# Performance work log

Hardware: AMD Instinct MI355X
Metric: run time of the kernel (lower is better)

## Reference

```python
import jax, jax.numpy as jnp
import numpy as np
import math

B, T, INP_DIM, OUT_DIM = 2, 4096, 1, 64
DEPTH, D_MODEL, N_HEADS, D_FF = 4, 512, 8, 2048
D_HEAD = D_MODEL // N_HEADS
EPS = 1e-5


def setup_inputs() -> dict:
    key = jax.random.key(0)
    ks = jax.random.split(key, 16)
    s = 0.02
    inp = {
        "x_in": jax.random.normal(ks[0], (B, T, INP_DIM), dtype=jnp.float32),
        "inp_w": jax.random.normal(ks[1], (INP_DIM, D_MODEL), dtype=jnp.float32) * s,
        "inp_b": jnp.zeros((D_MODEL,), dtype=jnp.float32),
        "pos_emb": jax.random.normal(ks[2], (T, D_MODEL), dtype=jnp.float32) * s,
        "ln1_g": jnp.ones((DEPTH, D_MODEL), dtype=jnp.float32),
        "ln1_b": jnp.zeros((DEPTH, D_MODEL), dtype=jnp.float32),
        "qkv_w": jax.random.normal(ks[3], (DEPTH, D_MODEL, 3 * D_MODEL), dtype=jnp.float32) * s,
        "proj_w": jax.random.normal(ks[4], (DEPTH, D_MODEL, D_MODEL), dtype=jnp.float32) * s,
        "ln2_g": jnp.ones((DEPTH, D_MODEL), dtype=jnp.float32),
        "ln2_b": jnp.zeros((DEPTH, D_MODEL), dtype=jnp.float32),
        "fc1_w": jax.random.normal(ks[5], (DEPTH, D_MODEL, D_FF), dtype=jnp.float32) * s,
        "fc2_w": jax.random.normal(ks[6], (DEPTH, D_FF, D_MODEL), dtype=jnp.float32) * s,
        "lnf_g": jnp.ones((D_MODEL,), dtype=jnp.float32),
        "lnf_b": jnp.zeros((D_MODEL,), dtype=jnp.float32),
        "head_w": jax.random.normal(ks[7], (D_MODEL, OUT_DIM), dtype=jnp.float32) * s,
        "head_b": jnp.zeros((OUT_DIM,), dtype=jnp.float32),
    }
    return inp


def _layernorm(x, g, b):
    mu = jnp.mean(x, axis=-1, keepdims=True)
    var = jnp.mean(jnp.square(x - mu), axis=-1, keepdims=True)
    return (x - mu) * jax.lax.rsqrt(var + EPS) * g + b


def _attn(x, qkv_w, proj_w):
    Bx, Tx, d = x.shape
    qkv = x @ qkv_w  # [B,T,3d]
    q, k, v = jnp.split(qkv, 3, axis=-1)
    q = q.reshape(Bx, Tx, N_HEADS, D_HEAD)
    k = k.reshape(Bx, Tx, N_HEADS, D_HEAD)
    v = v.reshape(Bx, Tx, N_HEADS, D_HEAD)
    scores = jnp.einsum('bqhd,bkhd->bhqk', q, k) / math.sqrt(D_HEAD)
    causal = jnp.tril(jnp.ones((Tx, Tx), dtype=bool))
    scores = jnp.where(causal, scores, -jnp.inf)
    attn = jax.nn.softmax(scores, axis=-1)
    out = jnp.einsum('bhqk,bkhd->bqhd', attn, v).reshape(Bx, Tx, d)
    return out @ proj_w


def reference(x_in, inp_w, inp_b, pos_emb, ln1_g, ln1_b, qkv_w, proj_w,
              ln2_g, ln2_b, fc1_w, fc2_w, lnf_g, lnf_b, head_w, head_b):
    x = x_in @ inp_w + inp_b + pos_emb[None, :, :]  # [B,T,d]
    for l in range(DEPTH):
        x = x + _attn(_layernorm(x, ln1_g[l], ln1_b[l]), qkv_w[l], proj_w[l])
        h = _layernorm(x, ln2_g[l], ln2_b[l])
        h = jax.nn.gelu(h @ fc1_w[l], approximate=False) @ fc2_w[l]
        x = x + h
    h = _layernorm(x, lnf_g, lnf_b)
    return h @ head_w + head_b  # [B,T,out_dim]
```

## Files before the change

### kernel.cpp

```cpp
#include <hip/hip_runtime.h>
#include <math.h>

typedef unsigned short u16;
typedef unsigned int u32;

#define B_ 2
#define T_ 4096
#define DM 512
#define NH 8
#define DH 64
#define DFF 2048
#define MTOT (B_*T_)

#define SCALEQ 0.18033688011112042f

using f32x4  = __attribute__((ext_vector_type(4))) float;
using f32x16 = __attribute__((ext_vector_type(16))) float;
using bf16x8 = __attribute__((ext_vector_type(8))) short;

__device__ __forceinline__ float b2f(u16 u) {
  union { u32 u; float f; } v; v.u = ((u32)u) << 16; return v.f;
}
__device__ __forceinline__ u16 f2b(float f) {
  union { float f; u32 u; } v; v.f = f;
  u32 r = v.u + 0x7FFFu + ((v.u >> 16) & 1u);
  return (u16)(r >> 16);
}
__device__ __forceinline__ u32 cvtpk(float lo, float hi) {
  u32 r;
  asm("v_cvt_pk_bf16_f32 %0, %1, %2" : "=v"(r) : "v"(lo), "v"(hi));
  return r;
}
#if __has_builtin(__builtin_amdgcn_exp2f)
#define EXP2(x) __builtin_amdgcn_exp2f(x)
#else
#define EXP2(x) __expf((x) * 0.6931471805599453f)
#endif
#if __has_builtin(__builtin_amdgcn_rcpf)
#define RCP(x) __builtin_amdgcn_rcpf(x)
#else
#define RCP(x) (1.0f / (x))
#endif

__device__ __forceinline__ void gload_lds(const u16* g, u16* l) {
  __builtin_amdgcn_global_load_lds(
      (const __attribute__((address_space(1))) void*)g,
      (__attribute__((address_space(3))) void*)l, 16, 0, 0);
}

__device__ __forceinline__ int lsw(int row, int col) {
  int slot = ((col >> 3) + (row >> 3) + 2 * (row & 7)) & 7;
  return (row << 6) + (slot << 3) + (col & 7);
}

__global__ __launch_bounds__(256) void embed_k(
    const float* __restrict__ x_in, const float* __restrict__ w,
    const float* __restrict__ bias, const float* __restrict__ pos,
    float* __restrict__ x) {
  int idx = blockIdx.x * 256 + threadIdx.x;
  int row = idx >> 9, d = idx & 511;
  int t = row & (T_ - 1);
  x[idx] = x_in[row] * w[d] + bias[d] + pos[t * DM + d];
}

__global__ __launch_bounds__(256) void ln_k(
    const float* __restrict__ x, const float* __restrict__ g,
    const float* __restrict__ bet, u16* __restrict__ y) {
  int wid = threadIdx.x >> 6, lane = threadIdx.x & 63;
  int row = blockIdx.x * 4 + wid;
  const float* xr = x + (size_t)row * DM + lane * 8;
  float4 a0 = *(const float4*)xr;
  float4 a1 = *(const float4*)(xr + 4);
  float v[8] = {a0.x, a0.y, a0.z, a0.w, a1.x, a1.y, a1.z, a1.w};
  float s = 0.f;
#pragma unroll
  for (int j = 0; j < 8; j++) s += v[j];
#pragma unroll
  for (int off = 32; off; off >>= 1) s += __shfl_xor(s, off);
  float mu = s * (1.0f / DM);
  float q = 0.f;
#pragma unroll
  for (int j = 0; j < 8; j++) { float e = v[j] - mu; q += e * e; }
#pragma unroll
  for (int off = 32; off; off >>= 1) q += __shfl_xor(q, off);
  float rs = rsqrtf(q * (1.0f / DM) + 1e-5f);
  float4 g0 = *(const float4*)(g + lane * 8);
  float4 g1 = *(const float4*)(g + lane * 8 + 4);
  float4 p0 = *(const float4*)(bet + lane * 8);
  float4 p1 = *(const float4*)(bet + lane * 8 + 4);
  float gg[8] = {g0.x, g0.y, g0.z, g0.w, g1.x, g1.y, g1.z, g1.w};
  float pp[8] = {p0.x, p0.y, p0.z, p0.w, p1.x, p1.y, p1.z, p1.w};
  uint4 st;
  st.x = cvtpk((v[0]-mu)*rs*gg[0]+pp[0], (v[1]-mu)*rs*gg[1]+pp[1]);
  st.y = cvtpk((v[2]-mu)*rs*gg[2]+pp[2], (v[3]-mu)*rs*gg[3]+pp[3]);
  st.z = cvtpk((v[4]-mu)*rs*gg[4]+pp[4], (v[5]-mu)*rs*gg[5]+pp[5]);
  st.w = cvtpk((v[6]-mu)*rs*gg[6]+pp[6], (v[7]-mu)*rs*gg[7]+pp[7]);
  *(uint4*)(y + (size_t)row * DM + lane * 8) = st;
}

__global__ __launch_bounds__(256) void wconv_k(
    const float* __restrict__ W, u16* __restrict__ Wt, int K, int N) {
  __shared__ float tile[32][33];
  const float* Wl = W + (size_t)blockIdx.z * K * N;
  u16* Wtl = Wt + (size_t)blockIdx.z * K * N;
  int k0 = blockIdx.x * 32, n0 = blockIdx.y * 32;
  int r = threadIdx.x >> 3, c4 = (threadIdx.x & 7) * 4;
  *(float4*)&tile[r][c4] = *(const float4*)(Wl + (size_t)(k0 + r) * N + n0 + c4);
  __syncthreads();
  uint2 st;
  st.x = cvtpk(tile[c4 + 0][r], tile[c4 + 1][r]);
  st.y = cvtpk(tile[c4 + 2][r], tile[c4 + 3][r]);
  *(uint2*)(Wtl + (size_t)(n0 + r) * K + k0 + c4) = st;
}

template<int EPI>
__global__ __launch_bounds__(256) void gemm_k(
    const u16* __restrict__ A, const u16* __restrict__ Bt,
    u16* __restrict__ Cb, float* __restrict__ Cf,
    int M, int N, int K, int scale_cols) {
  __shared__ u16 As[2][128][32];
  __shared__ u16 Bs[2][128][32];
  int tid = threadIdx.x;
  int lane = tid & 63, wid = tid >> 6;
  int wr = wid >> 1, wc = wid & 1;
  int m0 = blockIdx.y * 128, n0 = blockIdx.x * 128;
  f32x4 acc[4][4] = {};
  int rsub = lane >> 2, ksub = (lane & 3) * 8;
  const u16* Ab = A  + (size_t)(m0 + wid * 32 + rsub) * K + ksub;
  const u16* Bb = Bt + (size_t)(n0 + wid * 32 + rsub) * K + ksub;
#define GSTAGE(BUF, KO) { \
    gload_lds(Ab + (KO), &As[BUF][wid * 32][0]); \
    gload_lds(Ab + (size_t)16 * K + (KO), &As[BUF][wid * 32 + 16][0]); \
    gload_lds(Bb + (KO), &Bs[BUF][wid * 32][0]); \
    gload_lds(Bb + (size_t)16 * K + (KO), &Bs[BUF][wid * 32 + 16][0]); }
  GSTAGE(0, 0);
  __syncthreads();
  int r = lane & 15, kc = (lane >> 4) * 8;
  for (int k0 = 0; k0 < K; k0 += 32) {
    int cur = (k0 >> 5) & 1;
    if (k0 + 32 < K) GSTAGE(cur ^ 1, k0 + 32);
    bf16x8 af[4], bfr[4];
#pragma unroll
    for (int m = 0; m < 4; m++) af[m]  = *(const bf16x8*)&As[cur][wr*64 + m*16 + r][kc];
#pragma unroll
    for (int n = 0; n < 4; n++) bfr[n] = *(const bf16x8*)&Bs[cur][wc*64 + n*16 + r][kc];
#pragma unroll
    for (int m = 0; m < 4; m++)
#pragma unroll
      for (int n = 0; n < 4; n++)
        acc[m][n] = __builtin_amdgcn_mfma_f32_16x16x32_bf16(af[m], bfr[n], acc[m][n], 0, 0, 0);
    __syncthreads();
  }
  int r4 = (lane >> 4) * 4, cN = lane & 15;
#pragma unroll
  for (int m = 0; m < 4; m++) {
#pragma unroll
    for (int n = 0; n < 4; n++) {
      int col = n0 + wc*64 + n*16 + cN;
#pragma unroll
      for (int i = 0; i < 4; i++) {
        int row = m0 + wr*64 + m*16 + r4 + i;
        size_t off = (size_t)row * N + col;
        float v = acc[m][n][i];
        if (EPI == 0) {
          if (col < scale_cols) v *= SCALEQ;
          Cb[off] = f2b(v);
        } else if (EPI == 1) {
          Cf[off] += v;
        } else {
          float e = EXP2(v * (2.3022082f + 0.10294324f * v * v));
          Cb[off] = f2b(v * (1.0f - RCP(e + 1.0f)));
        }
      }
    }
  }
}

__global__ __launch_bounds__(256) void attn_k(const u16* __restrict__ qkv,
                                              u16* __restrict__ Opart,
                                              float* __restrict__ ml) {
  __shared__ u16 Ks[2][64 * 64];
  __shared__ u16 Vt[2][64 * 64];
  int tid = threadIdx.x;
  int w = tid >> 6, l = tid & 63;
  int hh = l >> 5, c = l & 31;
  int flat = blockIdx.y * 80 + blockIdx.x;
  int swz = (flat & 7) * 160 + (flat >> 3);
  int bh = swz / 80, slot = swz - bh * 80;
  int qb, ck, nc;
  if (slot < 8)       { qb = slot;                 ck = 0;                nc = 1; }
  else if (slot < 24) { int s = slot - 8;  qb = 8 + (s >> 1);  ck = s & 1; nc = 2; }
  else if (slot < 48) { int s = slot - 24; qb = 16 + s / 3;    ck = s - (qb - 16) * 3; nc = 3; }
  else                { int s = slot - 48; qb = 24 + (s >> 2); ck = s & 3; nc = 4; }
  int ntot = 2 * qb + 2;
  int kt0 = ck * ntot / nc, kt1 = (ck + 1) * ntot / nc;
  int b = bh >> 3, hd = bh & 7;
  int q0w = qb * 128 + w * 32;
  int q_abs = q0w + c;
  size_t base = (size_t)b * T_ * 1536;
  bf16x8 qf[4];
  const u16* qp = qkv + base + (size_t)q_abs * 1536 + hd * 64 + hh * 8;
#pragma unroll
  for (int kk = 0; kk < 4; kk++) qf[kk] = *(const bf16x8*)(qp + kk * 16);
  f32x16 oa0 = {}, oa1 = {};
  float m_run = -1e30f, l_run = 0.f;
  int sp = tid >> 3, d8 = (tid & 7) * 8;
  int r0 = sp * 2, r1 = r0 + 1;
  const u16* kvbase = qkv + base + DM + hd * 64 + d8;
  uint4 kreg0, kreg1, vreg0, vreg1;
#define AGLOAD(KT) { \
    const u16* s0_ = kvbase + (size_t)((KT) * 64 + r0) * 1536; \
    kreg0 = *(const uint4*)s0_; vreg0 = *(const uint4*)(s0_ + DM); \
    const u16* s1_ = s0_ + 1536; \
    kreg1 = *(const uint4*)s1_; vreg1 = *(const uint4*)(s1_ + DM); }
  AGLOAD(kt0);
  for (int kt = kt0; kt < kt1; kt++) {
    u16* Kb = Ks[kt & 1];
    u16* Vb = Vt[kt & 1];
    *(uint4*)&Kb[lsw(r0, d8)] = kreg0;
    *(uint4*)&Kb[lsw(r1, d8)] = kreg1;
    {
      const u16* v0 = (const u16*)&vreg0;
      const u16* v1 = (const u16*)&vreg1;
#pragma unroll
      for (int j = 0; j < 8; j++) {
        u32 pw = (u32)v0[j] | ((u32)v1[j] << 16);
        *(u32*)&Vb[lsw(d8 + j, r0)] = pw;
      }
    }
    if (kt + 1 < kt1) AGLOAD(kt + 1);
    __syncthreads();
    if (kt * 64 > q0w + 31) continue;
    bool needMask = (kt * 64 + 63 > q0w);
    f32x16 sa0 = {}, sa1 = {};
#pragma unroll
    for (int kk = 0; kk < 4; kk++) {
      bf16x8 ka  = *(const bf16x8*)&Kb[lsw(c,      kk * 16 + hh * 8)];
      bf16x8 kb2 = *(const bf16x8*)&Kb[lsw(32 + c, kk * 16 + hh * 8)];
      sa0 = __builtin_amdgcn_mfma_f32_32x32x16_bf16(ka,  qf[kk], sa0, 0, 0, 0);
      sa1 = __builtin_amdgcn_mfma_f32_32x32x16_bf16(kb2, qf[kk], sa1, 0, 0, 0);
    }
    if (needMask) {
#pragma unroll
      for (int g = 0; g < 4; g++)
#pragma unroll
        for (int i = 0; i < 4; i++) {
          int krow = kt * 64 + g * 8 + hh * 4 + i;
          if (krow > q_abs)      sa0[g * 4 + i] = -1e30f;
          if (krow + 32 > q_abs) sa1[g * 4 + i] = -1e30f;
        }
    }
    float pm = -1e30f;
#pragma unroll
    for (int r = 0; r < 16; r++) pm = fmaxf(pm, fmaxf(sa0[r], sa1[r]));
    pm = fmaxf(pm, __shfl_xor(pm, 32));
    if (!__all(pm - m_run <= 8.0f)) {
      float mnew = fmaxf(m_run, pm);
      float corr = EXP2(m_run - mnew);
      l_run *= corr;
#pragma unroll
      for (int r = 0; r < 16; r++) { oa0[r] *= corr; oa1[r] *= corr; }
      m_run = mnew;
    }
    float lsum = 0.f;
#pragma unroll
    for (int r = 0; r < 16; r++) {
      float e0 = EXP2(sa0[r] - m_run); sa0[r] = e0;
      float e1 = EXP2(sa1[r] - m_run); sa1[r] = e1;
      lsum += e0 + e1;
    }
    lsum += __shfl_xor(lsum, 32);
    l_run += lsum;
    u32 Aw[8], Bw_[8], Asw[8], Bsw[8];
#pragma unroll
    for (int r2 = 0; r2 < 4; r2++) {
      Aw[r2]      = cvtpk(sa0[4 * r2 + 0], sa0[4 * r2 + 1]);
      Bw_[r2]     = cvtpk(sa0[4 * r2 + 2], sa0[4 * r2 + 3]);
      Aw[4 + r2]  = cvtpk(sa1[4 * r2 + 0], sa1[4 * r2 + 1]);
      Bw_[4 + r2] = cvtpk(sa1[4 * r2 + 2], sa1[4 * r2 + 3]);
    }
#pragma unroll
    for (int i = 0; i < 8; i++) {
      Asw[i] = __shfl_xor(Aw[i], 32);
      Bsw[i] = __shfl_xor(Bw_[i], 32);
    }
#pragma unroll
    for (int ks = 0; ks < 4; ks++) {
      int mo = (ks >> 1) * 4;
      int r2e = mo + 2 * (ks & 1), r2o = r2e + 1;
      union { u32 wd[4]; bf16x8 v; } u;
      u.wd[0] = hh ? Asw[r2o] : Aw[r2e];
      u.wd[1] = hh ? Bsw[r2o] : Bw_[r2e];
      u.wd[2] = hh ? Aw[r2o]  : Asw[r2e];
      u.wd[3] = hh ? Bw_[r2o] : Bsw[r2e];
      bf16x8 va = *(const bf16x8*)&Vb[lsw(c,      ks * 16 + hh * 8)];
      bf16x8 vb = *(const bf16x8*)&Vb[lsw(32 + c, ks * 16 + hh * 8)];
      oa0 = __builtin_amdgcn_mfma_f32_32x32x16_bf16(va, u.v, oa0, 0, 0, 0);
      oa1 = __builtin_amdgcn_mfma_f32_32x32x16_bf16(vb, u.v, oa1, 0, 0, 0);
    }
  }
  int sidx = bh * 80 + slot;
  u16* op = Opart + ((size_t)sidx * 128 + w * 32 + c) * 64;
#pragma unroll
  for (int g = 0; g < 4; g++) {
    uint2 s0, s1;
    s0.x = cvtpk(oa0[4*g+0], oa0[4*g+1]);
    s0.y = cvtpk(oa0[4*g+2], oa0[4*g+3]);
    s1.x = cvtpk(oa1[4*g+0], oa1[4*g+1]);
    s1.y = cvtpk(oa1[4*g+2], oa1[4*g+3]);
    int d0 = g * 8 + hh * 4;
    *(uint2*)(op + d0)      = s0;
    *(uint2*)(op + 32 + d0) = s1;
  }
  if (hh == 0) {
    float2 p; p.x = m_run; p.y = l_run;
    *(float2*)&ml[((size_t)sidx * 128 + w * 32 + c) * 2] = p;
  }
}

__global__ __launch_bounds__(256) void comb_k(
    const u16* __restrict__ Opart, const float* __restrict__ ml,
    u16* __restrict__ attno) {
  int g = blockIdx.x * 256 + threadIdx.x;
  int d = g & 63, bhq = g >> 6;
  int bh = bhq >> 12, q = bhq & 4095;
  int qb = q >> 7, ri = q & 127;
  int bs, nc;
  if (qb < 8)       { bs = qb;                  nc = 1; }
  else if (qb < 16) { bs = 8 + ((qb - 8) << 1); nc = 2; }
  else if (qb < 24) { bs = 24 + (qb - 16) * 3;  nc = 3; }
  else              { bs = 48 + ((qb - 24) << 2); nc = 4; }
  int s0 = bh * 80 + bs;
  float m[4], lv[4], M = -1e30f;
  for (int cc = 0; cc < nc; cc++) {
    float2 p = *(const float2*)&ml[((size_t)(s0 + cc) * 128 + ri) * 2];
    m[cc] = p.x; lv[cc] = p.y;
    M = fmaxf(M, p.x);
  }
  float O = 0.f, L = 0.f;
  for (int cc = 0; cc < nc; cc++) {
    float wgt = EXP2(m[cc] - M);
    L += lv[cc] * wgt;
    O += b2f(Opart[((size_t)(s0 + cc) * 128 + ri) * 64 + d]) * wgt;
  }
  int b = bh >> 3, hd = bh & 7;
  attno[((size_t)b * T_ + q) * DM + hd * 64 + d] = f2b(O / L);
}

__global__ __launch_bounds__(256) void head_k(
    const u16* __restrict__ xb, const float* __restrict__ W,
    const float* __restrict__ bias, float* __restrict__ out) {
  int wid = threadIdx.x >> 6, lane = threadIdx.x & 63;
  int row = blockIdx.x * 4 + wid;
  const u16* xr = xb + (size_t)row * DM;
  float a0 = 0.f, a1 = 0.f, a2 = 0.f, a3 = 0.f;
  for (int d = 0; d < DM; d += 8) {
    uint4 xv = *(const uint4*)(xr + d);
    const u16* xp = (const u16*)&xv;
    const float* Wp = W + (size_t)d * 64 + lane;
    a0 += b2f(xp[0]) * Wp[0];
    a1 += b2f(xp[1]) * Wp[64];
    a2 += b2f(xp[2]) * Wp[128];
    a3 += b2f(xp[3]) * Wp[192];
    a0 += b2f(xp[4]) * Wp[256];
    a1 += b2f(xp[5]) * Wp[320];
    a2 += b2f(xp[6]) * Wp[384];
    a3 += b2f(xp[7]) * Wp[448];
  }
  out[(size_t)row * 64 + lane] = a0 + a1 + a2 + a3 + bias[lane];
}

extern "C" void kernel_launch(void* const* d_in, const int* in_sizes, int n_in,
                              void* d_out, int out_size, void* d_ws, size_t ws_size,
                              hipStream_t stream) {
  (void)in_sizes; (void)n_in; (void)out_size; (void)ws_size;
  const float* x_in  = (const float*)d_in[0];
  const float* inp_w = (const float*)d_in[1];
  const float* inp_b = (const float*)d_in[2];
  const float* pos   = (const float*)d_in[3];
  const float* ln1g  = (const float*)d_in[4];
  const float* ln1b  = (const float*)d_in[5];
  const float* qkvw  = (const float*)d_in[6];
  const float* projw = (const float*)d_in[7];
  const float* ln2g  = (const float*)d_in[8];
  const float* ln2b  = (const float*)d_in[9];
  const float* fc1w  = (const float*)d_in[10];
  const float* fc2w  = (const float*)d_in[11];
  const float* lnfg  = (const float*)d_in[12];
  const float* lnfb  = (const float*)d_in[13];
  const float* headw = (const float*)d_in[14];
  const float* headb = (const float*)d_in[15];

  char* ws = (char*)d_ws;
  size_t off = 0;
  float* x     = (float*)(ws + off); off += (size_t)MTOT * DM * 4;
  u16*  lnb    = (u16*)(ws + off);   off += (size_t)MTOT * DM * 2;
  u16*  qkvb   = (u16*)(ws + off);   off += (size_t)MTOT * 3 * DM * 2;
  u16*  attno  = (u16*)(ws + off);   off += (size_t)MTOT * DM * 2;
  u16*  ff     = qkvb;
  u16*  qkvt   = (u16*)(ws + off);   off += (size_t)4 * DM * 3 * DM * 2;
  u16*  projt  = (u16*)(ws + off);   off += (size_t)4 * DM * DM * 2;
  u16*  fc1t   = (u16*)(ws + off);   off += (size_t)4 * DM * DFF * 2;
  u16*  fc2t   = (u16*)(ws + off);   off += (size_t)4 * DFF * DM * 2;
  u16*  Opart  = (u16*)(ws + off);   off += (size_t)16 * 80 * 128 * 64 * 2;
  float* mlbuf = (float*)(ws + off); off += (size_t)16 * 80 * 128 * 2 * 4;

  wconv_k<<<dim3(16, 48, 4), 256, 0, stream>>>(qkvw,  qkvt, DM, 3 * DM);
  wconv_k<<<dim3(16, 16, 4), 256, 0, stream>>>(projw, projt, DM, DM);
  wconv_k<<<dim3(16, 64, 4), 256, 0, stream>>>(fc1w,  fc1t, DM, DFF);
  wconv_k<<<dim3(64, 16, 4), 256, 0, stream>>>(fc2w,  fc2t, DFF, DM);

  embed_k<<<(MTOT * DM) / 256, 256, 0, stream>>>(x_in, inp_w, inp_b, pos, x);
  for (int ly = 0; ly < 4; ly++) {
    ln_k<<<MTOT / 4, 256, 0, stream>>>(x, ln1g + ly * DM, ln1b + ly * DM, lnb);
    gemm_k<0><<<dim3(12, 64), 256, 0, stream>>>(lnb, qkvt + (size_t)ly * DM * 3 * DM,
                                                qkvb, nullptr, MTOT, 3 * DM, DM, DM);
    attn_k<<<dim3(80, 16), 256, 0, stream>>>(qkvb, Opart, mlbuf);
    comb_k<<<(16 * 4096 * 64) / 256, 256, 0, stream>>>(Opart, mlbuf, attno);
    gemm_k<1><<<dim3(4, 64), 256, 0, stream>>>(attno, projt + (size_t)ly * DM * DM,
                                               nullptr, x, MTOT, DM, DM, 0);
    ln_k<<<MTOT / 4, 256, 0, stream>>>(x, ln2g + ly * DM, ln2b + ly * DM, lnb);
    gemm_k<2><<<dim3(16, 64), 256, 0, stream>>>(lnb, fc1t + (size_t)ly * DM * DFF,
                                                ff, nullptr, MTOT, DFF, DM, 0);
    gemm_k<1><<<dim3(4, 64), 256, 0, stream>>>(ff, fc2t + (size_t)ly * DFF * DM,
                                               nullptr, x, MTOT, DM, DFF, 0);
  }
  ln_k<<<MTOT / 4, 256, 0, stream>>>(x, lnfg, lnfb, lnb);
  head_k<<<MTOT / 4, 256, 0, stream>>>(lnb, headw, headb, (float*)d_out);
}
```

Baseline: 1.045 ms.

## Split-K fc2 into partial buffers fused into next layernorm; rebalance attention chunks

```diff
diff --git a/kernel.cpp b/kernel.cpp
--- a/kernel.cpp
+++ b/kernel.cpp
@@ -63,15 +63,31 @@
   x[idx] = x_in[row] * w[d] + bias[d] + pos[t * DM + d];
 }
 
+template<int NP>
 __global__ __launch_bounds__(256) void ln_k(
-    const float* __restrict__ x, const float* __restrict__ g,
-    const float* __restrict__ bet, u16* __restrict__ y) {
+    float* __restrict__ x, const float* __restrict__ P,
+    const float* __restrict__ g, const float* __restrict__ bet,
+    u16* __restrict__ y) {
   int wid = threadIdx.x >> 6, lane = threadIdx.x & 63;
   int row = blockIdx.x * 4 + wid;
-  const float* xr = x + (size_t)row * DM + lane * 8;
+  float* xr = x + (size_t)row * DM + lane * 8;
   float4 a0 = *(const float4*)xr;
   float4 a1 = *(const float4*)(xr + 4);
   float v[8] = {a0.x, a0.y, a0.z, a0.w, a1.x, a1.y, a1.z, a1.w};
+  if (NP > 0) {
+#pragma unroll
+    for (int s = 0; s < NP; s++) {
+      const float* pr = P + (size_t)s * MTOT * DM + (size_t)row * DM + lane * 8;
+      float4 p0 = *(const float4*)pr;
+      float4 p1 = *(const float4*)(pr + 4);
+      v[0] += p0.x; v[1] += p0.y; v[2] += p0.z; v[3] += p0.w;
+      v[4] += p1.x; v[5] += p1.y; v[6] += p1.z; v[7] += p1.w;
+    }
+    float4 w0; w0.x = v[0]; w0.y = v[1]; w0.z = v[2]; w0.w = v[3];
+    float4 w1; w1.x = v[4]; w1.y = v[5]; w1.z = v[6]; w1.w = v[7];
+    *(float4*)xr = w0;
+    *(float4*)(xr + 4) = w1;
+  }
   float s = 0.f;
 #pragma unroll
   for (int j = 0; j < 8; j++) s += v[j];
@@ -117,17 +133,19 @@
 __global__ __launch_bounds__(256) void gemm_k(
     const u16* __restrict__ A, const u16* __restrict__ Bt,
     u16* __restrict__ Cb, float* __restrict__ Cf,
-    int M, int N, int K, int scale_cols) {
+    int M, int N, int K, int Kslice, int scale_cols) {
   __shared__ u16 As[2][128][32];
   __shared__ u16 Bs[2][128][32];
   int tid = threadIdx.x;
   int lane = tid & 63, wid = tid >> 6;
   int wr = wid >> 1, wc = wid & 1;
   int m0 = blockIdx.y * 128, n0 = blockIdx.x * 128;
+  int kbeg = blockIdx.z * Kslice;
+  if (EPI == 3) Cf += (size_t)blockIdx.z * M * N;
   f32x4 acc[4][4] = {};
   int rsub = lane >> 2, ksub = (lane & 3) * 8;
-  const u16* Ab = A  + (size_t)(m0 + wid * 32 + rsub) * K + ksub;
-  const u16* Bb = Bt + (size_t)(n0 + wid * 32 + rsub) * K + ksub;
+  const u16* Ab = A  + (size_t)(m0 + wid * 32 + rsub) * K + kbeg + ksub;
+  const u16* Bb = Bt + (size_t)(n0 + wid * 32 + rsub) * K + kbeg + ksub;
 #define GSTAGE(BUF, KO) { \
     gload_lds(Ab + (KO), &As[BUF][wid * 32][0]); \
     gload_lds(Ab + (size_t)16 * K + (KO), &As[BUF][wid * 32 + 16][0]); \
@@ -136,9 +154,9 @@
   GSTAGE(0, 0);
   __syncthreads();
   int r = lane & 15, kc = (lane >> 4) * 8;
-  for (int k0 = 0; k0 < K; k0 += 32) {
+  for (int k0 = 0; k0 < Kslice; k0 += 32) {
     int cur = (k0 >> 5) & 1;
-    if (k0 + 32 < K) GSTAGE(cur ^ 1, k0 + 32);
+    if (k0 + 32 < Kslice) GSTAGE(cur ^ 1, k0 + 32);
     bf16x8 af[4], bfr[4];
 #pragma unroll
     for (int m = 0; m < 4; m++) af[m]  = *(const bf16x8*)&As[cur][wr*64 + m*16 + r][kc];
@@ -167,6 +185,8 @@
           Cb[off] = f2b(v);
         } else if (EPI == 1) {
           Cf[off] += v;
+        } else if (EPI == 3) {
+          Cf[off] = v;
         } else {
           float e = EXP2(v * (2.3022082f + 0.10294324f * v * v));
           Cb[off] = f2b(v * (1.0f - RCP(e + 1.0f)));
@@ -184,16 +204,17 @@
   int tid = threadIdx.x;
   int w = tid >> 6, l = tid & 63;
   int hh = l >> 5, c = l & 31;
-  int flat = blockIdx.y * 80 + blockIdx.x;
-  int swz = (flat & 7) * 160 + (flat >> 3);
-  int bh = swz / 80, slot = swz - bh * 80;
-  int qb, ck, nc;
-  if (slot < 8)       { qb = slot;                 ck = 0;                nc = 1; }
-  else if (slot < 24) { int s = slot - 8;  qb = 8 + (s >> 1);  ck = s & 1; nc = 2; }
-  else if (slot < 48) { int s = slot - 24; qb = 16 + s / 3;    ck = s - (qb - 16) * 3; nc = 3; }
-  else                { int s = slot - 48; qb = 24 + (s >> 2); ck = s & 3; nc = 4; }
+  int flat = blockIdx.y * 144 + blockIdx.x;
+  int swz = (flat & 7) * 288 + (flat >> 3);
+  int bh = swz / 144, slot = swz - bh * 144;
+  int g = 0;
+  while (2 * (g + 1) * (g + 2) <= slot) g++;
+  int s2 = slot - 2 * g * (g + 1);
+  int qb = 4 * g + s2 / (g + 1);
+  int ck = s2 - (s2 / (g + 1)) * (g + 1);
   int ntot = 2 * qb + 2;
-  int kt0 = ck * ntot / nc, kt1 = (ck + 1) * ntot / nc;
+  int kt0 = ck * 8;
+  int kt1 = kt0 + 8 < ntot ? kt0 + 8 : ntot;
   int b = bh >> 3, hd = bh & 7;
   int q0w = qb * 128 + w * 32;
   int q_abs = q0w + c;
@@ -233,6 +254,7 @@
     if (kt * 64 > q0w + 31) continue;
     bool needMask = (kt * 64 + 63 > q0w);
     f32x16 sa0 = {}, sa1 = {};
+    __builtin_amdgcn_s_setprio(1);
 #pragma unroll
     for (int kk = 0; kk < 4; kk++) {
       bf16x8 ka  = *(const bf16x8*)&Kb[lsw(c,      kk * 16 + hh * 8)];
@@ -240,14 +262,15 @@
       sa0 = __builtin_amdgcn_mfma_f32_32x32x16_bf16(ka,  qf[kk], sa0, 0, 0, 0);
       sa1 = __builtin_amdgcn_mfma_f32_32x32x16_bf16(kb2, qf[kk], sa1, 0, 0, 0);
     }
+    __builtin_amdgcn_s_setprio(0);
     if (needMask) {
 #pragma unroll
-      for (int g = 0; g < 4; g++)
+      for (int gi = 0; gi < 4; gi++)
 #pragma unroll
         for (int i = 0; i < 4; i++) {
-          int krow = kt * 64 + g * 8 + hh * 4 + i;
-          if (krow > q_abs)      sa0[g * 4 + i] = -1e30f;
-          if (krow + 32 > q_abs) sa1[g * 4 + i] = -1e30f;
+          int krow = kt * 64 + gi * 8 + hh * 4 + i;
+          if (krow > q_abs)      sa0[gi * 4 + i] = -1e30f;
+          if (krow + 32 > q_abs) sa1[gi * 4 + i] = -1e30f;
         }
     }
     float pm = -1e30f;
@@ -284,6 +307,7 @@
       Asw[i] = __shfl_xor(Aw[i], 32);
       Bsw[i] = __shfl_xor(Bw_[i], 32);
     }
+    __builtin_amdgcn_s_setprio(1);
 #pragma unroll
     for (int ks = 0; ks < 4; ks++) {
       int mo = (ks >> 1) * 4;
@@ -298,17 +322,18 @@
       oa0 = __builtin_amdgcn_mfma_f32_32x32x16_bf16(va, u.v, oa0, 0, 0, 0);
       oa1 = __builtin_amdgcn_mfma_f32_32x32x16_bf16(vb, u.v, oa1, 0, 0, 0);
     }
-  }
-  int sidx = bh * 80 + slot;
+    __builtin_amdgcn_s_setprio(0);
+  }
+  int sidx = bh * 144 + slot;
   u16* op = Opart + ((size_t)sidx * 128 + w * 32 + c) * 64;
 #pragma unroll
-  for (int g = 0; g < 4; g++) {
+  for (int gi = 0; gi < 4; gi++) {
     uint2 s0, s1;
-    s0.x = cvtpk(oa0[4*g+0], oa0[4*g+1]);
-    s0.y = cvtpk(oa0[4*g+2], oa0[4*g+3]);
-    s1.x = cvtpk(oa1[4*g+0], oa1[4*g+1]);
-    s1.y = cvtpk(oa1[4*g+2], oa1[4*g+3]);
-    int d0 = g * 8 + hh * 4;
+    s0.x = cvtpk(oa0[4*gi+0], oa0[4*gi+1]);
+    s0.y = cvtpk(oa0[4*gi+2], oa0[4*gi+3]);
+    s1.x = cvtpk(oa1[4*gi+0], oa1[4*gi+1]);
+    s1.y = cvtpk(oa1[4*gi+2], oa1[4*gi+3]);
+    int d0 = gi * 8 + hh * 4;
     *(uint2*)(op + d0)      = s0;
     *(uint2*)(op + 32 + d0) = s1;
   }
@@ -321,26 +346,22 @@
 __global__ __launch_bounds__(256) void comb_k(
     const u16* __restrict__ Opart, const float* __restrict__ ml,
     u16* __restrict__ attno) {
-  int g = blockIdx.x * 256 + threadIdx.x;
-  int d = g & 63, bhq = g >> 6;
+  int gi = blockIdx.x * 256 + threadIdx.x;
+  int d = gi & 63, bhq = gi >> 6;
   int bh = bhq >> 12, q = bhq & 4095;
   int qb = q >> 7, ri = q & 127;
-  int bs, nc;
-  if (qb < 8)       { bs = qb;                  nc = 1; }
-  else if (qb < 16) { bs = 8 + ((qb - 8) << 1); nc = 2; }
-  else if (qb < 24) { bs = 24 + (qb - 16) * 3;  nc = 3; }
-  else              { bs = 48 + ((qb - 24) << 2); nc = 4; }
-  int s0 = bh * 80 + bs;
-  float m[4], lv[4], M = -1e30f;
+  int g = qb >> 2;
+  int nc = g + 1;
+  int bs = 2 * g * (g + 1) + (qb & 3) * (g + 1);
+  int s0 = bh * 144 + bs;
+  float M = -1e30f;
+  for (int cc = 0; cc < nc; cc++)
+    M = fmaxf(M, ml[((size_t)(s0 + cc) * 128 + ri) * 2]);
+  float O = 0.f, L = 0.f;
   for (int cc = 0; cc < nc; cc++) {
     float2 p = *(const float2*)&ml[((size_t)(s0 + cc) * 128 + ri) * 2];
-    m[cc] = p.x; lv[cc] = p.y;
-    M = fmaxf(M, p.x);
-  }
-  float O = 0.f, L = 0.f;
-  for (int cc = 0; cc < nc; cc++) {
-    float wgt = EXP2(m[cc] - M);
-    L += lv[cc] * wgt;
+    float wgt = EXP2(p.x - M);
+    L += p.y * wgt;
     O += b2f(Opart[((size_t)(s0 + cc) * 128 + ri) * 64 + d]) * wgt;
   }
   int b = bh >> 3, hd = bh & 7;
@@ -402,8 +423,10 @@
   u16*  projt  = (u16*)(ws + off);   off += (size_t)4 * DM * DM * 2;
   u16*  fc1t   = (u16*)(ws + off);   off += (size_t)4 * DM * DFF * 2;
   u16*  fc2t   = (u16*)(ws + off);   off += (size_t)4 * DFF * DM * 2;
-  u16*  Opart  = (u16*)(ws + off);   off += (size_t)16 * 80 * 128 * 64 * 2;
-  float* mlbuf = (float*)(ws + off); off += (size_t)16 * 80 * 128 * 2 * 4;
+  char* shared = ws + off;
+  u16*  Opart  = (u16*)shared;
+  float* mlbuf = (float*)(shared + (size_t)16 * 144 * 128 * 64 * 2);
+  float* fcp   = (float*)shared;
 
   wconv_k<<<dim3(16, 48, 4), 256, 0, stream>>>(qkvw,  qkvt, DM, 3 * DM);
   wconv_k<<<dim3(16, 16, 4), 256, 0, stream>>>(projw, projt, DM, DM);
@@ -412,19 +435,22 @@
 
   embed_k<<<(MTOT * DM) / 256, 256, 0, stream>>>(x_in, inp_w, inp_b, pos, x);
   for (int ly = 0; ly < 4; ly++) {
-    ln_k<<<MTOT / 4, 256, 0, stream>>>(x, ln1g + ly * DM, ln1b + ly * DM, lnb);
+    if (ly == 0)
+      ln_k<0><<<MTOT / 4, 256, 0, stream>>>(x, nullptr, ln1g, ln1b, lnb);
+    else
+      ln_k<2><<<MTOT / 4, 256, 0, stream>>>(x, fcp, ln1g + ly * DM, ln1b + ly * DM, lnb);
     gemm_k<0><<<dim3(12, 64), 256, 0, stream>>>(lnb, qkvt + (size_t)ly * DM * 3 * DM,
-                                                qkvb, nullptr, MTOT, 3 * DM, DM, DM);
-    attn_k<<<dim3(80, 16), 256, 0, stream>>>(qkvb, Opart, mlbuf);
+                                                qkvb, nullptr, MTOT, 3 * DM, DM, DM, DM);
+    attn_k<<<dim3(144, 16), 256, 0, stream>>>(qkvb, Opart, mlbuf);
     comb_k<<<(16 * 4096 * 64) / 256, 256, 0, stream>>>(Opart, mlbuf, attno);
     gemm_k<1><<<dim3(4, 64), 256, 0, stream>>>(attno, projt + (size_t)ly * DM * DM,
-                                               nullptr, x, MTOT, DM, DM, 0);
-    ln_k<<<MTOT / 4, 256, 0, stream>>>(x, ln2g + ly * DM, ln2b + ly * DM, lnb);
+                                               nullptr, x, MTOT, DM, DM, DM, 0);
+    ln_k<0><<<MTOT / 4, 256, 0, stream>>>(x, nullptr, ln2g + ly * DM, ln2b + ly * DM, lnb);
     gemm_k<2><<<dim3(16, 64), 256, 0, stream>>>(lnb, fc1t + (size_t)ly * DM * DFF,
-                                                ff, nullptr, MTOT, DFF, DM, 0);
-    gemm_k<1><<<dim3(4, 64), 256, 0, stream>>>(ff, fc2t + (size_t)ly * DFF * DM,
-                                               nullptr, x, MTOT, DM, DFF, 0);
-  }
-  ln_k<<<MTOT / 4, 256, 0, stream>>>(x, lnfg, lnfb, lnb);
+                                                ff, nullptr, MTOT, DFF, DM, DM, 0);
+    gemm_k<3><<<dim3(4, 64, 2), 256, 0, stream>>>(ff, fc2t + (size_t)ly * DFF * DM,
+                                                  nullptr, fcp, MTOT, DM, DFF, DFF / 2, 0);
+  }
+  ln_k<2><<<MTOT / 4, 256, 0, stream>>>(x, fcp, lnfg, lnfb, lnb);
   head_k<<<MTOT / 4, 256, 0, stream>>>(lnb, headw, headb, (float*)d_out);
 }
```

New measurement: 1.025 ms. -2.0%, faster.
